# Kernel optimization log

Measured on AMD Instinct MI355X. Metric: run time of the kernel, lower is better.

Reference implementation:

```python
import jax, jax.numpy as jnp
import numpy as np

B, S, D = 2, 2048, 1024
H, L = 16, 512
DH = D // H
LN_EPS = 1e-5


def setup_inputs() -> dict:
    key = jax.random.key(0)
    ks = jax.random.split(key, 6)
    w = 0.02  # init scale for weights
    return {
        "x": jax.random.normal(ks[0], (B, S, D), jnp.float32),
        "W_q": jax.random.normal(ks[1], (D, D), jnp.float32) * w,
        "W_dkv": jax.random.normal(ks[2], (L, D), jnp.float32) * w,
        "W_uk": jax.random.normal(ks[3], (D, L), jnp.float32) * w,
        "W_uv": jax.random.normal(ks[4], (D, L), jnp.float32) * w,
        "W_o": jax.random.normal(ks[5], (D, D), jnp.float32) * w,
        "ln_gamma": jnp.ones((L,), jnp.float32),
        "ln_beta": jnp.zeros((L,), jnp.float32),
    }


def reference(x, W_q, W_dkv, W_uk, W_uv, W_o, ln_gamma, ln_beta):
    # latent KV: LayerNorm(x @ W_dkv^T)  -> [B, S, L]
    c = x @ W_dkv.T
    mu = jnp.mean(c, axis=-1, keepdims=True)
    var = jnp.mean((c - mu) ** 2, axis=-1, keepdims=True)
    c_kv = (c - mu) * jax.lax.rsqrt(var + LN_EPS) * ln_gamma + ln_beta

    # absorbed key projection: (W_q @ W_uk) viewed per head  -> [H, DH, L]
    absorbed_k = (W_q @ W_uk).reshape(H, DH, L)

    # q is raw x reshaped per head (W_q absorbed)  -> [B, S, H, DH]
    q = x.reshape(B, S, H, DH)
    tmp = jnp.einsum('bshd,hdl->bhsl', q, absorbed_k)         # [B,H,S,L]
    scores = jnp.einsum('bhsl,btl->bhst', tmp, c_kv) / np.sqrt(DH)

    # causal mask (past_length = 0, no kv_cache -> S_full == S)
    mask = jnp.tril(jnp.ones((S, S), bool))
    scores = jnp.where(mask[None, None], scores, -1e30)
    attn = jax.nn.softmax(scores, axis=-1)                    # [B,H,S,S]

    # values decompressed from latent  -> [B, S, H, DH]
    v = (c_kv @ W_uv.T).reshape(B, S, H, DH)
    ctx = jnp.einsum('bhst,bthd->bshd', attn, v).reshape(B, S, D)
    out = ctx @ W_o.T
    return out, c_kv
```

## Files before the change

kernel.cpp:

```cpp
#include <hip/hip_runtime.h>


typedef __attribute__((ext_vector_type(4))) float f32x4;
typedef __attribute__((ext_vector_type(8))) unsigned short u16x8;
typedef __attribute__((ext_vector_type(4))) unsigned short u16x4;
typedef __attribute__((ext_vector_type(8))) __bf16 bf16x8;

__device__ __forceinline__ unsigned short f2bf(float f) {
  unsigned int u = __builtin_bit_cast(unsigned int, f);
  u += 0x7FFFu + ((u >> 16) & 1u);
  return (unsigned short)(u >> 16);
}
__device__ __forceinline__ unsigned short f2bf_rz(float f) {
  return (unsigned short)(__builtin_bit_cast(unsigned int, f) >> 16);
}

__device__ __forceinline__ f32x4 mfma16(u16x8 a, u16x8 b, f32x4 c) {
  return __builtin_amdgcn_mfma_f32_16x16x32_bf16(
      __builtin_bit_cast(bf16x8, a), __builtin_bit_cast(bf16x8, b), c, 0, 0, 0);
}

__device__ __forceinline__ void gload_lds16(const void* g, void* l) {
  __builtin_amdgcn_global_load_lds(
      (const __attribute__((address_space(1))) unsigned int*)g,
      (__attribute__((address_space(3))) unsigned int*)l, 16, 0, 0);
}

__global__ __launch_bounds__(256)
void fused_cvt(const float* __restrict__ x, unsigned short* __restrict__ xb,
               const float* __restrict__ wq, unsigned short* __restrict__ wqb,
               const float* __restrict__ wdkv, unsigned short* __restrict__ wdkvb,
               const float* __restrict__ wuv, unsigned short* __restrict__ wuvb,
               const float* __restrict__ wo, unsigned short* __restrict__ wob) {
  const int total = 1048576 + 262144 + 131072 + 131072 + 262144;
  for (int i = blockIdx.x * 256 + threadIdx.x; i < total; i += gridDim.x * 256) {
    const float* src; unsigned short* dst; int off;
    if (i < 1048576)      { src = x;    dst = xb;    off = i; }
    else if (i < 1310720) { src = wq;   dst = wqb;   off = i - 1048576; }
    else if (i < 1441792) { src = wdkv; dst = wdkvb; off = i - 1310720; }
    else if (i < 1572864) { src = wuv;  dst = wuvb;  off = i - 1441792; }
    else                  { src = wo;   dst = wob;   off = i - 1572864; }
    float4 v = ((const float4*)src)[off];
    u16x4 o;
    o[0] = f2bf(v.x); o[1] = f2bf(v.y); o[2] = f2bf(v.z); o[3] = f2bf(v.w);
    ((u16x4*)dst)[off] = o;
  }
}

__global__ __launch_bounds__(256) void transpose_cvt(const float* __restrict__ in,
                                                     unsigned short* __restrict__ out) {
  __shared__ float t[64][65];
  int r0 = blockIdx.y * 64, c0 = blockIdx.x * 64;
  int lr = threadIdx.x >> 4, lc = (threadIdx.x & 15) * 4;
#pragma unroll
  for (int i = 0; i < 4; i++) {
    int row = lr + i * 16;
    float4 v = *(const float4*)(in + (size_t)(r0 + row) * 512 + c0 + lc);
    t[row][lc] = v.x; t[row][lc + 1] = v.y; t[row][lc + 2] = v.z; t[row][lc + 3] = v.w;
  }
  __syncthreads();
#pragma unroll
  for (int i = 0; i < 4; i++) {
    int oc = lr + i * 16;
    u16x4 o;
    o[0] = f2bf(t[lc + 0][oc]); o[1] = f2bf(t[lc + 1][oc]);
    o[2] = f2bf(t[lc + 2][oc]); o[3] = f2bf(t[lc + 3][oc]);
    *(u16x4*)(out + (size_t)(c0 + oc) * 1024 + r0 + lc) = o;
  }
}

template <int MODE, int IM, int JF, int MINW>
__global__ __launch_bounds__(256, MINW)
void gemm_bt(const unsigned short* __restrict__ A, const unsigned short* __restrict__ B,
             void* __restrict__ C1, void* __restrict__ C2,
             int M, int N, int K, int lda, int ldb, int ldc) {
  constexpr int BM = IM * 32, BN = JF * 32;
  __shared__ __align__(16) unsigned short sA[2][BM * 64];
  __shared__ __align__(16) unsigned short sB[2][BN * 64];
  const int tid = threadIdx.x;
  const int w = tid >> 6, ln = tid & 63;
  const int m0 = blockIdx.y * BM, n0 = blockIdx.x * BN;
  const int wm = (w >> 1) * (IM * 16), wn = (w & 1) * (JF * 16);
  const int c16 = ln & 15, g = ln >> 4;
  f32x4 zero = {0.f, 0.f, 0.f, 0.f};
  f32x4 acc[IM][JF];
#pragma unroll
  for (int i = 0; i < IM; i++)
#pragma unroll
    for (int j = 0; j < JF; j++) acc[i][j] = zero;

#define STAGE_G(kt, bf)                                                        \
  {                                                                            \
    _Pragma("unroll") for (int l = 0; l < BM / 32; l++) {                      \
      int c = l * 256 + tid;                                                   \
      int row = c >> 3, pc = c & 7;                                            \
      gload_lds16(A + (size_t)(m0 + row) * lda + (kt) + ((pc ^ (row & 7)) << 3),\
                  (char*)&sA[bf][0] + (l * 256 + w * 64) * 16);                \
    }                                                                          \
    _Pragma("unroll") for (int l = 0; l < BN / 32; l++) {                      \
      int c = l * 256 + tid;                                                   \
      int row = c >> 3, pc = c & 7;                                            \
      gload_lds16(B + (size_t)(n0 + row) * ldb + (kt) + ((pc ^ (row & 7)) << 3),\
                  (char*)&sB[bf][0] + (l * 256 + w * 64) * 16);                \
    }                                                                          \
  }

  STAGE_G(0, 0);
  __syncthreads();
  int bf = 0;
  for (int kt = 0; kt < K; kt += 64) {
    if (kt + 64 < K) STAGE_G(kt + 64, bf ^ 1);
    u16x8 af[IM][2], bfr[JF][2];
#pragma unroll
    for (int i = 0; i < IM; i++) {
      int ra = wm + i * 16 + c16;
#pragma unroll
      for (int kk = 0; kk < 2; kk++)
        af[i][kk] = *(const u16x8*)((const char*)&sA[bf][0] + ra * 128 +
                                    ((((kk << 2) + g) ^ (ra & 7)) << 4));
    }
#pragma unroll
    for (int j = 0; j < JF; j++) {
      int rb = wn + j * 16 + c16;
#pragma unroll
      for (int kk = 0; kk < 2; kk++)
        bfr[j][kk] = *(const u16x8*)((const char*)&sB[bf][0] + rb * 128 +
                                     ((((kk << 2) + g) ^ (rb & 7)) << 4));
    }
#pragma unroll
    for (int kk = 0; kk < 2; kk++)
#pragma unroll
      for (int i = 0; i < IM; i++)
#pragma unroll
        for (int j = 0; j < JF; j++)
          acc[i][j] = mfma16(af[i][kk], bfr[j][kk], acc[i][j]);
    __syncthreads();
    bf ^= 1;
  }
#undef STAGE_G
  const int row0 = m0 + wm + g * 4;
  const int col0 = n0 + wn + c16;
  if (MODE == 1) {
    float* C = (float*)C1;
#pragma unroll
    for (int i = 0; i < IM; i++)
#pragma unroll
      for (int j = 0; j < JF; j++)
#pragma unroll
        for (int r = 0; r < 4; r++)
          C[(size_t)(row0 + i * 16 + r) * ldc + col0 + j * 16] = acc[i][j][r];
  } else if (MODE == 0) {
    unsigned short* C = (unsigned short*)C1;
#pragma unroll
    for (int i = 0; i < IM; i++)
#pragma unroll
      for (int j = 0; j < JF; j++)
#pragma unroll
        for (int r = 0; r < 4; r++)
          C[(size_t)(row0 + i * 16 + r) * ldc + col0 + j * 16] = f2bf(acc[i][j][r]);
  } else {
    if (n0 < 1024) {
      unsigned short* C = (unsigned short*)C1;
#pragma unroll
      for (int i = 0; i < IM; i++)
#pragma unroll
        for (int j = 0; j < JF; j++)
#pragma unroll
          for (int r = 0; r < 4; r++)
            C[(size_t)(row0 + i * 16 + r) * ldc + col0 + j * 16] = f2bf(acc[i][j][r]);
    } else {
      unsigned short* C = (unsigned short*)C2;
#pragma unroll
      for (int i = 0; i < IM; i++)
#pragma unroll
        for (int j = 0; j < JF; j++) {
          u16x4 t4;
#pragma unroll
          for (int r = 0; r < 4; r++) t4[r] = f2bf(acc[i][j][r]);
          *(u16x4*)(C + (size_t)(col0 + j * 16 - 1024) * 4096 + row0 + i * 16) = t4;
        }
    }
  }
}

__global__ __launch_bounds__(256)
void ln_rows(const float* __restrict__ cin, const float* __restrict__ gamma,
             const float* __restrict__ beta, float* __restrict__ of32,
             unsigned short* __restrict__ obf) {
  int row = blockIdx.x * 4 + (threadIdx.x >> 6);
  int ln = threadIdx.x & 63;
  const float* r = cin + (size_t)row * 512 + ln * 8;
  float4 a = *(const float4*)r;
  float4 b = *(const float4*)(r + 4);
  float xv[8] = {a.x, a.y, a.z, a.w, b.x, b.y, b.z, b.w};
  float s = 0.f, q = 0.f;
#pragma unroll
  for (int j = 0; j < 8; j++) { s += xv[j]; q += xv[j] * xv[j]; }
#pragma unroll
  for (int m = 1; m < 64; m <<= 1) { s += __shfl_xor(s, m); q += __shfl_xor(q, m); }
  float mu = s * (1.f / 512.f);
  float var = q * (1.f / 512.f) - mu * mu;
  float rs = rsqrtf(var + 1e-5f);
  float gm[8], bt[8];
  *(float4*)&gm[0] = *(const float4*)(gamma + ln * 8);
  *(float4*)&gm[4] = *(const float4*)(gamma + ln * 8 + 4);
  *(float4*)&bt[0] = *(const float4*)(beta + ln * 8);
  *(float4*)&bt[4] = *(const float4*)(beta + ln * 8 + 4);
  float o[8];
#pragma unroll
  for (int j = 0; j < 8; j++) o[j] = (xv[j] - mu) * rs * gm[j] + bt[j];
  float4 o0 = {o[0], o[1], o[2], o[3]}, o1 = {o[4], o[5], o[6], o[7]};
  *(float4*)(of32 + (size_t)row * 512 + ln * 8) = o0;
  *(float4*)(of32 + (size_t)row * 512 + ln * 8 + 4) = o1;
  u16x8 ob;
#pragma unroll
  for (int j = 0; j < 8; j++) ob[j] = f2bf(o[j]);
  *(u16x8*)(obf + (size_t)row * 512 + ln * 8) = ob;
}

__global__ __launch_bounds__(256, 3)
void mla_attn4(const unsigned short* __restrict__ kabs,
               const unsigned short* __restrict__ xq,
               const unsigned short* __restrict__ vT,
               unsigned short* __restrict__ ctx) {
  __shared__ __align__(16) unsigned short sK[2][64 * 64];
  __shared__ __align__(16) unsigned short sVT[2][64 * 64];
  __shared__ __align__(16) unsigned short sP[4][16 * 72];
  const int tid = threadIdx.x, w = tid >> 6, ln = tid & 63;
  const int g = ln >> 4, c16 = ln & 15;
  const int b = blockIdx.y >> 4, h = blockIdx.y & 15;
  const int qb = 31 - blockIdx.x;
  const int q0 = qb * 64;
  const int qw = q0 + w * 16;
  const size_t rowb = (size_t)b * 2048;

  u16x8 qf[2];
  {
    const unsigned short* qp = xq + (rowb + qw + c16) * 1024 + h * 64 + g * 8;
    qf[0] = *(const u16x8*)(qp);
    qf[1] = *(const u16x8*)(qp + 32);
  }
  f32x4 zero = {0.f, 0.f, 0.f, 0.f};
  f32x4 o[4] = {zero, zero, zero, zero};
  float lsum[4] = {0.f, 0.f, 0.f, 0.f};
  const float SC = 0.18033688011112042f;
  const float M0 = 8.f;
  unsigned short* Pw = &sP[w][0];
  const unsigned short* kb_g = kabs + rowb * 1024 + h * 64;
  const unsigned short* vb_g = vT + (size_t)(h * 64) * 4096 + rowb;
  const int ntile = qb + 1;

#define STAGE_A(tt, bfi)                                                       \
  {                                                                            \
    int t0s = (tt) * 64;                                                       \
    _Pragma("unroll") for (int l = 0; l < 2; l++) {                            \
      int c = l * 256 + tid;                                                   \
      int row = c >> 3, pc = c & 7;                                            \
      gload_lds16(kb_g + (size_t)(t0s + row) * 1024 + ((pc ^ (row & 7)) << 3), \
                  (char*)&sK[bfi][0] + (l * 256 + w * 64) * 16);               \
    }                                                                          \
    _Pragma("unroll") for (int l = 0; l < 2; l++) {                            \
      int c = l * 256 + tid;                                                   \
      int row = c >> 3, pc = c & 7;                                            \
      gload_lds16(vb_g + (size_t)row * 4096 + t0s + ((pc ^ (row & 7)) << 3),   \
                  (char*)&sVT[bfi][0] + (l * 256 + w * 64) * 16);              \
    }                                                                          \
  }

  STAGE_A(0, 0);
  __syncthreads();
  int bf = 0;
  for (int tt = 0; tt < ntile; tt++) {
    const int t0 = tt * 64;
    if (tt + 1 < ntile) STAGE_A(tt + 1, bf ^ 1);
    f32x4 s[4];
#pragma unroll
    for (int nt = 0; nt < 4; nt++) {
      int t = nt * 16 + c16;
      int sw = t & 7;
      const char* kb = (const char*)&sK[bf][0] + t * 128;
      f32x4 a = zero;
      a = mfma16(qf[0], *(const u16x8*)(kb + ((g ^ sw) << 4)), a);
      a = mfma16(qf[1], *(const u16x8*)(kb + (((4 + g) ^ sw) << 4)), a);
      s[nt] = a;
    }
    if (t0 + 63 <= qw) {
#pragma unroll
      for (int nt = 0; nt < 4; nt++)
#pragma unroll
        for (int r = 0; r < 4; r++) {
          float p = exp2f(s[nt][r] * SC - M0);
          lsum[r] += p;
          s[nt][r] = p;
        }
    } else {
#pragma unroll
      for (int nt = 0; nt < 4; nt++) {
        int tcol = t0 + nt * 16 + c16;
#pragma unroll
        for (int r = 0; r < 4; r++) {
          float p = (tcol <= qw + g * 4 + r) ? exp2f(s[nt][r] * SC - M0) : 0.f;
          lsum[r] += p;
          s[nt][r] = p;
        }
      }
    }
#pragma unroll
    for (int nt = 0; nt < 4; nt++)
#pragma unroll
      for (int r = 0; r < 4; r++)
        Pw[(g * 4 + r) * 72 + nt * 16 + c16] = f2bf_rz(s[nt][r]);
#pragma unroll
    for (int ks = 0; ks < 2; ks++) {
      u16x8 pa = *(const u16x8*)((const char*)Pw + c16 * 144 + ks * 64 + g * 16);
#pragma unroll
      for (int dt = 0; dt < 4; dt++) {
        int d = dt * 16 + c16;
        const char* vb = (const char*)&sVT[bf][0] + d * 128 +
                         ((((ks << 2) + g) ^ (d & 7)) << 4);
        o[dt] = mfma16(pa, *(const u16x8*)vb, o[dt]);
      }
    }
    __syncthreads();
    bf ^= 1;
  }
#undef STAGE_A
#pragma unroll
  for (int r = 0; r < 4; r++) {
    float t = lsum[r];
    t += __shfl_xor(t, 1); t += __shfl_xor(t, 2);
    t += __shfl_xor(t, 4); t += __shfl_xor(t, 8);
    float inv = 1.f / t;
    unsigned short* cp = ctx + (rowb + qw + g * 4 + r) * 1024 + h * 64 + c16;
#pragma unroll
    for (int dt = 0; dt < 4; dt++) cp[dt * 16] = f2bf(o[dt][r] * inv);
  }
}

extern "C" void kernel_launch(void* const* d_in, const int* in_sizes, int n_in,
                              void* d_out, int out_size, void* d_ws, size_t ws_size,
                              hipStream_t stream) {
  const float* x    = (const float*)d_in[0];
  const float* Wq   = (const float*)d_in[1];
  const float* Wdkv = (const float*)d_in[2];
  const float* Wuk  = (const float*)d_in[3];
  const float* Wuv  = (const float*)d_in[4];
  const float* Wo   = (const float*)d_in[5];
  const float* gam  = (const float*)d_in[6];
  const float* bet  = (const float*)d_in[7];
  float* out_f = (float*)d_out;
  float* ckv_f = out_f + (size_t)4096 * 1024;

  char* ws = (char*)d_ws;
  unsigned short* xb     = (unsigned short*)(ws);
  unsigned short* wq_b   = (unsigned short*)(ws + 8388608);
  unsigned short* wdkv_b = (unsigned short*)(ws + 10485760);
  unsigned short* wukT_b = (unsigned short*)(ws + 11534336);
  unsigned short* akt_b  = (unsigned short*)(ws + 12582912);
  unsigned short* wuv_b  = (unsigned short*)(ws + 13631488);
  unsigned short* wo_b   = (unsigned short*)(ws + 14680064);
  unsigned short* ckv_b  = (unsigned short*)(ws + 16777216);
  float*          c_f    = (float*)(ws + 20971520);
  unsigned short* kabs   = (unsigned short*)(ws + 29360128);
  unsigned short* vT     = (unsigned short*)(ws + 37748736);
  unsigned short* ctx_b  = (unsigned short*)(ws + 46137344);

  fused_cvt<<<2048, 256, 0, stream>>>(x, xb, Wq, wq_b, Wdkv, wdkv_b,
                                      Wuv, wuv_b, Wo, wo_b);
  transpose_cvt<<<dim3(8, 16), 256, 0, stream>>>(Wuk, wukT_b);

  gemm_bt<1, 2, 2, 4><<<dim3(8, 64), 256, 0, stream>>>(xb, wdkv_b, c_f, nullptr,
                                                       4096, 512, 1024, 1024, 1024, 512);
  ln_rows<<<1024, 256, 0, stream>>>(c_f, gam, bet, ckv_f, ckv_b);
  gemm_bt<0, 1, 2, 4><<<dim3(8, 32), 256, 0, stream>>>(wq_b, wukT_b, akt_b, nullptr,
                                                       1024, 512, 1024, 1024, 1024, 512);
  gemm_bt<3, 4, 4, 2><<<dim3(16, 32), 256, 0, stream>>>(ckv_b, akt_b, kabs, vT,
                                                        4096, 2048, 512, 512, 512, 1024);
  mla_attn4<<<dim3(32, 32), 256, 0, stream>>>(kabs, xb, vT, ctx_b);
  gemm_bt<1, 2, 4, 3><<<dim3(8, 64), 256, 0, stream>>>(ctx_b, wo_b, out_f, nullptr,
                                                       4096, 1024, 1024, 1024, 1024, 1024);
}
```

Measured before the change: 230.3 us.

## Split causal attention KV range into balanced chunks with combine pass

The attention kernel now splits each query block's key range into chunks of up to 8 tiles, so long causal rows are processed by several workgroups instead of one. This evens out per-block work and raises the grid from 1024 to 2560 workgroups. Each chunk writes its unnormalized partial output (bf16) and row sums to workspace, and a new combine kernel adds them and normalizes. The cost is an extra launch, extra global traffic for the partials, and an added bf16 rounding of the partial outputs. The combine is valid only because a fixed max offset is used instead of a running max.

```diff
diff --git a/kernel.cpp b/kernel.cpp
--- a/kernel.cpp
+++ b/kernel.cpp
@@ -13,6 +13,9 @@
 }
 __device__ __forceinline__ unsigned short f2bf_rz(float f) {
   return (unsigned short)(__builtin_bit_cast(unsigned int, f) >> 16);
+}
+__device__ __forceinline__ float bf2f(unsigned short u) {
+  return __builtin_bit_cast(float, (unsigned int)u << 16);
 }
 
 __device__ __forceinline__ f32x4 mfma16(u16x8 a, u16x8 b, f32x4 c) {
@@ -219,17 +222,25 @@
 }
 
 __global__ __launch_bounds__(256, 3)
-void mla_attn4(const unsigned short* __restrict__ kabs,
+void mla_attn5(const unsigned short* __restrict__ kabs,
                const unsigned short* __restrict__ xq,
                const unsigned short* __restrict__ vT,
-               unsigned short* __restrict__ ctx) {
+               unsigned short* __restrict__ Opart,
+               float* __restrict__ Lpart) {
   __shared__ __align__(16) unsigned short sK[2][64 * 64];
   __shared__ __align__(16) unsigned short sVT[2][64 * 64];
   __shared__ __align__(16) unsigned short sP[4][16 * 72];
   const int tid = threadIdx.x, w = tid >> 6, ln = tid & 63;
   const int g = ln >> 4, c16 = ln & 15;
-  const int b = blockIdx.y >> 4, h = blockIdx.y & 15;
-  const int qb = 31 - blockIdx.x;
+  const int bh = blockIdx.y;
+  const int b = bh >> 4, h = bh & 15;
+  int cid = blockIdx.x, qb, ch;
+  if (cid < 8)       { qb = cid;                 ch = 0; }
+  else if (cid < 24) { qb = 8 + ((cid - 8) >> 1);  ch = (cid - 8) & 1; }
+  else if (cid < 48) { qb = 16 + (cid - 24) / 3;   ch = (cid - 24) % 3; }
+  else               { qb = 24 + ((cid - 48) >> 2); ch = (cid - 48) & 3; }
+  const int ts = ch * 8;
+  const int te = min(ts + 8, qb + 1);
   const int q0 = qb * 64;
   const int qw = q0 + w * 16;
   const size_t rowb = (size_t)b * 2048;
@@ -248,7 +259,6 @@
   unsigned short* Pw = &sP[w][0];
   const unsigned short* kb_g = kabs + rowb * 1024 + h * 64;
   const unsigned short* vb_g = vT + (size_t)(h * 64) * 4096 + rowb;
-  const int ntile = qb + 1;
 
 #define STAGE_A(tt, bfi)                                                       \
   {                                                                            \
@@ -267,12 +277,12 @@
     }                                                                          \
   }
 
-  STAGE_A(0, 0);
+  STAGE_A(ts, 0);
   __syncthreads();
   int bf = 0;
-  for (int tt = 0; tt < ntile; tt++) {
+  for (int tt = ts; tt < te; tt++) {
     const int t0 = tt * 64;
-    if (tt + 1 < ntile) STAGE_A(tt + 1, bf ^ 1);
+    if (tt + 1 < te) STAGE_A(tt + 1, bf ^ 1);
     f32x4 s[4];
 #pragma unroll
     for (int nt = 0; nt < 4; nt++) {
@@ -325,16 +335,53 @@
     bf ^= 1;
   }
 #undef STAGE_A
+  unsigned short* op = Opart + ((size_t)bh * 80 + cid) * 4096;
+  float* lp = Lpart + ((size_t)bh * 80 + cid) * 64;
 #pragma unroll
   for (int r = 0; r < 4; r++) {
     float t = lsum[r];
     t += __shfl_xor(t, 1); t += __shfl_xor(t, 2);
     t += __shfl_xor(t, 4); t += __shfl_xor(t, 8);
-    float inv = 1.f / t;
-    unsigned short* cp = ctx + (rowb + qw + g * 4 + r) * 1024 + h * 64 + c16;
-#pragma unroll
-    for (int dt = 0; dt < 4; dt++) cp[dt * 16] = f2bf(o[dt][r] * inv);
-  }
+    int ql = w * 16 + g * 4 + r;
+    if (c16 == 0) lp[ql] = t;
+#pragma unroll
+    for (int dt = 0; dt < 4; dt++)
+      op[ql * 64 + dt * 16 + c16] = f2bf(o[dt][r]);
+  }
+}
+
+__global__ __launch_bounds__(256)
+void attn_combine(const unsigned short* __restrict__ Opart,
+                  const float* __restrict__ Lpart,
+                  unsigned short* __restrict__ ctx) {
+  const int qb = blockIdx.x, bh = blockIdx.y;
+  const int b = bh >> 4, h = bh & 15;
+  const int ncq = (qb >> 3) + 1;
+  const int g8 = qb >> 3;
+  const int start = (g8 == 0 ? 0 : (g8 == 1 ? 8 : (g8 == 2 ? 24 : 48)));
+  const int cid0 = start + (qb & 7) * ncq;
+  const int q = threadIdx.x >> 2;
+  const int d0 = (threadIdx.x & 3) * 16;
+  float acc[16];
+#pragma unroll
+  for (int j = 0; j < 16; j++) acc[j] = 0.f;
+  float lacc = 0.f;
+  for (int c = 0; c < ncq; c++) {
+    size_t base = (size_t)bh * 80 + cid0 + c;
+    lacc += Lpart[base * 64 + q];
+    const unsigned short* op = Opart + base * 4096 + q * 64 + d0;
+    u16x8 v0 = *(const u16x8*)(op);
+    u16x8 v1 = *(const u16x8*)(op + 8);
+#pragma unroll
+    for (int j = 0; j < 8; j++) { acc[j] += bf2f(v0[j]); acc[8 + j] += bf2f(v1[j]); }
+  }
+  float inv = 1.f / lacc;
+  u16x8 o0, o1;
+#pragma unroll
+  for (int j = 0; j < 8; j++) { o0[j] = f2bf(acc[j] * inv); o1[j] = f2bf(acc[8 + j] * inv); }
+  unsigned short* cp = ctx + ((size_t)b * 2048 + qb * 64 + q) * 1024 + h * 64 + d0;
+  *(u16x8*)(cp) = o0;
+  *(u16x8*)(cp + 8) = o1;
 }
 
 extern "C" void kernel_launch(void* const* d_in, const int* in_sizes, int n_in,
@@ -364,6 +411,8 @@
   unsigned short* kabs   = (unsigned short*)(ws + 29360128);
   unsigned short* vT     = (unsigned short*)(ws + 37748736);
   unsigned short* ctx_b  = (unsigned short*)(ws + 46137344);
+  unsigned short* Opart  = (unsigned short*)(ws + 54525952);
+  float*          Lpart  = (float*)(ws + 75497472);
 
   fused_cvt<<<2048, 256, 0, stream>>>(x, xb, Wq, wq_b, Wdkv, wdkv_b,
                                       Wuv, wuv_b, Wo, wo_b);
@@ -376,7 +425,8 @@
                                                        1024, 512, 1024, 1024, 1024, 512);
   gemm_bt<3, 4, 4, 2><<<dim3(16, 32), 256, 0, stream>>>(ckv_b, akt_b, kabs, vT,
                                                         4096, 2048, 512, 512, 512, 1024);
-  mla_attn4<<<dim3(32, 32), 256, 0, stream>>>(kabs, xb, vT, ctx_b);
+  mla_attn5<<<dim3(80, 32), 256, 0, stream>>>(kabs, xb, vT, Opart, Lpart);
+  attn_combine<<<dim3(32, 32), 256, 0, stream>>>(Opart, Lpart, ctx_b);
   gemm_bt<1, 2, 4, 3><<<dim3(8, 64), 256, 0, stream>>>(ctx_b, wo_b, out_f, nullptr,
                                                        4096, 1024, 1024, 1024, 1024, 1024);
 }
```

Result: faster. 205.0 us (-11.0%).
